# Optimization experiments

Measured on AMD Instinct MI355X. Metric: run time of the kernel, lower is better.

The kernel has to match this reference:

```python
import jax, jax.numpy as jnp
import numpy as np

B, CL, QL, D = 32, 1024, 512, 256


def setup_inputs() -> dict:
    key = jax.random.key(0)
    ks = jax.random.split(key, 8)
    c = jax.random.normal(ks[0], (B, CL, D), jnp.float32)
    q = jax.random.normal(ks[1], (B, QL, D), jnp.float32)
    scale = 1.0 / np.sqrt(D)
    w_c = jax.random.normal(ks[2], (D,), jnp.float32) * scale
    b_c = jax.random.normal(ks[3], (), jnp.float32) * 0.01
    w_q = jax.random.normal(ks[4], (D,), jnp.float32) * scale
    b_q = jax.random.normal(ks[5], (), jnp.float32) * 0.01
    w_cq = jax.random.normal(ks[6], (D,), jnp.float32) * scale
    b_cq = jax.random.normal(ks[7], (), jnp.float32) * 0.01
    return {"c": c, "q": q, "w_c": w_c, "b_c": b_c, "w_q": w_q, "b_q": b_q,
            "w_cq": w_cq, "b_cq": b_cq}


def reference(c, q, w_c, b_c, w_q, b_q, w_cq, b_cq):
    # s[b,i,j] = w_c.c_i + w_q.q_j + w_cq.(c_i*q_j) + biases
    sc = c @ w_c + b_c                                   # (B, CL)
    sq = q @ w_q + b_q                                   # (B, QL)
    # The original per-j loop att_weight_cq(c * q_j) is a batched bilinear form.
    cq = jnp.einsum('bid,bjd,d->bij', c, q, w_cq) + b_cq  # (B, CL, QL)
    s = sc[:, :, None] + sq[:, None, :] + cq              # (B, CL, QL)
    a = jax.nn.softmax(s, axis=2)
    c2q_att = jnp.einsum('bij,bjd->bid', a, q)            # (B, CL, D)
    bvec = jax.nn.softmax(jnp.max(s, axis=2), axis=1)     # (B, CL)
    q2c = jnp.einsum('bi,bid->bd', bvec, c)               # (B, D)
    q2c_att = jnp.broadcast_to(q2c[:, None, :], c.shape)  # (B, CL, D)
    x = jnp.concatenate([c, c2q_att, c * c2q_att, c * q2c_att], axis=-1)
    return x
```

## Files before the change

kernel.cpp:

```cpp
#include <hip/hip_runtime.h>

#define B_  32
#define CL_ 1024
#define QL_ 512
#define D_  256

typedef _Float16 f16;
typedef __attribute__((ext_vector_type(2))) _Float16 f16x2;
typedef __attribute__((ext_vector_type(4))) _Float16 f16x4;
typedef __attribute__((ext_vector_type(8))) _Float16 f16x8;
typedef __attribute__((ext_vector_type(4))) float    f32x4;

__global__ __launch_bounds__(256) void k0_prep(const float* __restrict__ q,
                                               const float* __restrict__ w_q,
                                               f16* __restrict__ q_h,
                                               f16* __restrict__ qT_h,
                                               float* __restrict__ sqv) {
  __shared__ f16 q_l[64][258];
  int b = blockIdx.y, j0 = blockIdx.x * 64, tid = threadIdx.x;
  int r = tid >> 2, seg = tid & 3;
  const float* qrow = q   + ((size_t)(b * QL_ + j0 + r)) * D_ + seg * 64;
  f16*        qhrow = q_h + ((size_t)(b * QL_ + j0 + r)) * D_ + seg * 64;
  float dot = 0.f;
  #pragma unroll
  for (int u = 0; u < 16; ++u) {
    f32x4 v  = *(const f32x4*)(qrow + 4 * u);
    f32x4 wv = *(const f32x4*)(w_q + seg * 64 + 4 * u);
    f16x4 h;
    h[0] = (f16)v[0]; h[1] = (f16)v[1]; h[2] = (f16)v[2]; h[3] = (f16)v[3];
    *(f16x4*)(&q_l[r][seg * 64 + 4 * u]) = h;
    *(f16x4*)(qhrow + 4 * u) = h;
    dot += v[0]*wv[0] + v[1]*wv[1] + v[2]*wv[2] + v[3]*wv[3];
  }
  dot += __shfl_xor(dot, 1, 64);
  dot += __shfl_xor(dot, 2, 64);
  if (seg == 0) sqv[b * QL_ + j0 + r] = dot;
  __syncthreads();
  f16* qTb = qT_h + (size_t)b * D_ * QL_ + j0;
  #pragma unroll
  for (int s = 0; s < 32; ++s) {
    int e = tid + 256 * s;
    int d = e >> 5, j2 = (e & 31) * 2;
    f16x2 p;
    p[0] = q_l[j2][d];
    p[1] = q_l[j2 + 1][d];
    *(f16x2*)(qTb + (size_t)d * QL_ + j2) = p;
  }
}

__global__ __launch_bounds__(512, 2) void k1_fused(
    const float* __restrict__ c, const f16* __restrict__ q_h,
    const f16* __restrict__ qT_h, const float* __restrict__ sqv,
    const float* __restrict__ w_c, const float* __restrict__ w_cq,
    float* __restrict__ out, float* __restrict__ mrow)
{
  __shared__ alignas(16) char smem[142848];
  f16 (*cw_t)[264]  = (f16 (*)[264])(smem);
  char* P_b         = smem;
  float (*o_l)[260] = (float (*)[260])(smem);
  float* sqv_l = (float*)(smem + 133120);
  float* wcq_l = (float*)(smem + 135168);
  float* wc_l  = (float*)(smem + 136192);
  float* scv_l = (float*)(smem + 137216);
  float (*red)[128] = (float (*)[128])(smem + 137728);
  float* mf = (float*)(smem + 141824);
  float* lf = (float*)(smem + 142336);

  const int tid = threadIdx.x;
  const int w = tid >> 6, l = tid & 63, g = l >> 4, l15 = l & 15;
  const int lin = blockIdx.x, xcd = lin & 7, slot = lin >> 3;
  const int b  = xcd * 4 + (slot >> 3);
  const int i0 = (slot & 7) * 128;

  if (tid < 256) { wcq_l[tid] = w_cq[tid]; wc_l[tid] = w_c[tid]; }
  sqv_l[tid] = sqv[b * QL_ + tid];
  __syncthreads();

  {
    int row = tid >> 2, seg = tid & 3;
    const float* crow = c + (size_t)(b * CL_ + i0 + row) * D_ + seg * 64;
    float dot = 0.f;
    #pragma unroll
    for (int u = 0; u < 16; ++u) {
      f32x4 v  = *(const f32x4*)(crow + 4 * u);
      f32x4 wv = *(const f32x4*)(wcq_l + seg * 64 + 4 * u);
      f32x4 w2 = *(const f32x4*)(wc_l  + seg * 64 + 4 * u);
      f16x4 h;
      h[0] = (f16)(v[0]*wv[0]); h[1] = (f16)(v[1]*wv[1]);
      h[2] = (f16)(v[2]*wv[2]); h[3] = (f16)(v[3]*wv[3]);
      *(f16x4*)(&cw_t[row][seg * 64 + 4 * u]) = h;
      dot += v[0]*w2[0] + v[1]*w2[1] + v[2]*w2[2] + v[3]*w2[3];
    }
    dot += __shfl_xor(dot, 1, 64); dot += __shfl_xor(dot, 2, 64);
    if (seg == 0) scv_l[row] = dot;
  }
  __syncthreads();

  f32x4 acc[8][4];
  #pragma unroll
  for (int fi = 0; fi < 8; ++fi)
    #pragma unroll
    for (int fj = 0; fj < 4; ++fj)
      acc[fi][fj] = (f32x4){0.f,0.f,0.f,0.f};

  const f16* qb = q_h + (size_t)b * QL_ * D_ + (size_t)(64 * w + l15) * D_ + 8 * g;
  #pragma unroll
  for (int dk = 0; dk < 8; ++dk) {
    f16x8 av[8];
    #pragma unroll
    for (int fi = 0; fi < 8; ++fi)
      av[fi] = *(const f16x8*)(&cw_t[16 * fi + l15][dk * 32 + 8 * g]);
    #pragma unroll
    for (int fj = 0; fj < 4; ++fj) {
      f16x8 bf = *(const f16x8*)(qb + (size_t)(16 * fj) * D_ + dk * 32);
      #pragma unroll
      for (int fi = 0; fi < 8; ++fi)
        acc[fi][fj] = __builtin_amdgcn_mfma_f32_16x16x32_f16(av[fi], bf, acc[fi][fj], 0, 0, 0);
    }
  }

  #pragma unroll
  for (int fi = 0; fi < 8; ++fi) {
    #pragma unroll
    for (int r = 0; r < 4; ++r) {
      float mx = -1e30f;
      #pragma unroll
      for (int fj = 0; fj < 4; ++fj) {
        float v = acc[fi][fj][r] + sqv_l[64 * w + 16 * fj + l15];
        acc[fi][fj][r] = v;
        mx = fmaxf(mx, v);
      }
      mx = fmaxf(mx, __shfl_xor(mx, 1, 64));
      mx = fmaxf(mx, __shfl_xor(mx, 2, 64));
      mx = fmaxf(mx, __shfl_xor(mx, 4, 64));
      mx = fmaxf(mx, __shfl_xor(mx, 8, 64));
      if (l15 == 0) red[w][16 * fi + 4 * g + r] = mx;
    }
  }
  __syncthreads();
  if (tid < 128) {
    float m = red[0][tid];
    #pragma unroll
    for (int w2 = 1; w2 < 8; ++w2) m = fmaxf(m, red[w2][tid]);
    mf[tid] = m;
    mrow[b * CL_ + i0 + tid] = m + scv_l[tid];
  }
  __syncthreads();
  #pragma unroll
  for (int fi = 0; fi < 8; ++fi) {
    #pragma unroll
    for (int r = 0; r < 4; ++r) {
      float mv = mf[16 * fi + 4 * g + r];
      float s = 0.f;
      #pragma unroll
      for (int fj = 0; fj < 4; ++fj) {
        float p = __expf(acc[fi][fj][r] - mv);
        acc[fi][fj][r] = p;
        s += p;
      }
      s += __shfl_xor(s, 1, 64); s += __shfl_xor(s, 2, 64);
      s += __shfl_xor(s, 4, 64); s += __shfl_xor(s, 8, 64);
      if (l15 == 0) red[w][16 * fi + 4 * g + r] = s;
    }
  }
  __syncthreads();
  if (tid < 128) {
    float s = 0.f;
    #pragma unroll
    for (int w2 = 0; w2 < 8; ++w2) s += red[w2][tid];
    lf[tid] = 1.0f / s;
  }
  __syncthreads();

  #pragma unroll
  for (int fi = 0; fi < 8; ++fi) {
    #pragma unroll
    for (int r = 0; r < 4; ++r) {
      int row = 16 * fi + 4 * g + r;
      float inv = lf[row];
      int rb = (row << 10) ^ ((row & 7) << 4);
      #pragma unroll
      for (int fj = 0; fj < 4; ++fj) {
        int byte = (rb ^ ((128 * w + 32 * fj + 2 * l15) & 0x70))
                 | ((128 * w + 32 * fj + 2 * l15) & ~0x70);
        *(f16*)(P_b + (((row << 10) + 128 * w + 32 * fj + 2 * l15) ^ ((row & 7) << 4)))
            = (f16)(acc[fi][fj][r] * inv);
        (void)byte;
      }
    }
  }
  __syncthreads();

  f32x4 o[8][2];
  #pragma unroll
  for (int fi = 0; fi < 8; ++fi) { o[fi][0] = (f32x4){0.f,0.f,0.f,0.f}; o[fi][1] = o[fi][0]; }
  const f16* qTb = qT_h + (size_t)b * D_ * QL_ + (size_t)(32 * w + l15) * QL_ + 8 * g;
  #pragma unroll
  for (int jt = 0; jt < 16; ++jt) {
    f16x8 qf0 = *(const f16x8*)(qTb + jt * 32);
    f16x8 qf1 = *(const f16x8*)(qTb + 16 * QL_ + jt * 32);
    #pragma unroll
    for (int fi = 0; fi < 8; ++fi) {
      int row = 16 * fi + l15;
      f16x8 pa = *(const f16x8*)(P_b + (((row << 10) + 64 * jt + 16 * g) ^ ((row & 7) << 4)));
      o[fi][0] = __builtin_amdgcn_mfma_f32_16x16x32_f16(pa, qf0, o[fi][0], 0, 0, 0);
      o[fi][1] = __builtin_amdgcn_mfma_f32_16x16x32_f16(pa, qf1, o[fi][1], 0, 0, 0);
    }
  }
  __syncthreads();

  #pragma unroll
  for (int fi = 0; fi < 8; ++fi)
    #pragma unroll
    for (int fd = 0; fd < 2; ++fd)
      #pragma unroll
      for (int r = 0; r < 4; ++r)
        o_l[16 * fi + 4 * g + r][32 * w + 16 * fd + l15] = o[fi][fd][r];
  __syncthreads();

  #pragma unroll
  for (int s = 0; s < 16; ++s) {
    int idx = tid + 512 * s;
    int row = idx >> 6, c4 = (idx & 63) * 4;
    size_t rowoff = (size_t)(b * CL_ + i0 + row);
    f32x4 c2q = *(const f32x4*)(&o_l[row][c4]);
    f32x4 cv  = *(const f32x4*)(c + rowoff * D_ + c4);
    f32x4 prod;
    prod[0] = cv[0]*c2q[0]; prod[1] = cv[1]*c2q[1];
    prod[2] = cv[2]*c2q[2]; prod[3] = cv[3]*c2q[3];
    float* ob = out + rowoff * (4 * D_) + c4;
    *(f32x4*)(ob)          = cv;
    *(f32x4*)(ob + D_)     = c2q;
    *(f32x4*)(ob + 2 * D_) = prod;
  }
}

__global__ __launch_bounds__(256) void k2a_bvec(const float* __restrict__ mrow,
                                                float* __restrict__ bvec) {
  __shared__ float red[256];
  int b = blockIdx.x, tid = threadIdx.x;
  f32x4 v = *(const f32x4*)(mrow + b * CL_ + tid * 4);
  float mx = fmaxf(fmaxf(v[0], v[1]), fmaxf(v[2], v[3]));
  red[tid] = mx;
  __syncthreads();
  for (int s = 128; s > 0; s >>= 1) {
    if (tid < s) red[tid] = fmaxf(red[tid], red[tid + s]);
    __syncthreads();
  }
  float gmx = red[0];
  __syncthreads();
  f32x4 e;
  e[0] = __expf(v[0] - gmx); e[1] = __expf(v[1] - gmx);
  e[2] = __expf(v[2] - gmx); e[3] = __expf(v[3] - gmx);
  red[tid] = e[0] + e[1] + e[2] + e[3];
  __syncthreads();
  for (int s = 128; s > 0; s >>= 1) {
    if (tid < s) red[tid] += red[tid + s];
    __syncthreads();
  }
  float inv = 1.0f / red[0];
  e[0] *= inv; e[1] *= inv; e[2] *= inv; e[3] *= inv;
  *(f32x4*)(bvec + b * CL_ + tid * 4) = e;
}

__global__ __launch_bounds__(256) void k2b_part(const float* __restrict__ c,
                                                const float* __restrict__ bvec,
                                                float* __restrict__ part) {
  __shared__ f32x4 pl[4][64];
  int ch = blockIdx.x, b = blockIdx.y, tid = threadIdx.x;
  int ro = tid >> 6, dl = tid & 63;
  const float* cb = c + ((size_t)b * CL_ + ch * 128) * D_;
  const float* bv = bvec + b * CL_ + ch * 128;
  f32x4 acc = (f32x4){0.f, 0.f, 0.f, 0.f};
  for (int i = ro; i < 128; i += 4) {
    float wgt = bv[i];
    f32x4 v = *(const f32x4*)(cb + (size_t)i * D_ + dl * 4);
    acc[0] += wgt * v[0]; acc[1] += wgt * v[1];
    acc[2] += wgt * v[2]; acc[3] += wgt * v[3];
  }
  pl[ro][dl] = acc;
  __syncthreads();
  if (tid < 64) {
    f32x4 s = (pl[0][tid] + pl[1][tid]) + (pl[2][tid] + pl[3][tid]);
    *(f32x4*)(part + ((size_t)(b * 8 + ch)) * D_ + tid * 4) = s;
  }
}

__global__ __launch_bounds__(256) void k2c_red(const float* __restrict__ part,
                                               float* __restrict__ q2c) {
  int b = blockIdx.x, d = threadIdx.x;
  float s = 0.f;
  #pragma unroll
  for (int ch = 0; ch < 8; ++ch) s += part[((size_t)(b * 8 + ch)) * D_ + d];
  q2c[b * D_ + d] = s;
}

__global__ __launch_bounds__(256) void k3_tail(const float* __restrict__ c,
                                               const float* __restrict__ q2c,
                                               float* __restrict__ out) {
  size_t idx = (size_t)blockIdx.x * 256 + threadIdx.x;
  int b   = (int)(idx >> 16);
  int rem = (int)(idx & 65535);
  int i = rem >> 6, d4 = (rem & 63) * 4;
  f32x4 cv = *(const f32x4*)(c + (size_t)(b * CL_ + i) * D_ + d4);
  f32x4 gv = *(const f32x4*)(q2c + b * D_ + d4);
  f32x4 r;
  r[0] = cv[0]*gv[0]; r[1] = cv[1]*gv[1]; r[2] = cv[2]*gv[2]; r[3] = cv[3]*gv[3];
  *(f32x4*)(out + (size_t)(b * CL_ + i) * (4 * D_) + 3 * D_ + d4) = r;
}

extern "C" void kernel_launch(void* const* d_in, const int* in_sizes, int n_in,
                              void* d_out, int out_size, void* d_ws, size_t ws_size,
                              hipStream_t stream) {
  const float* c    = (const float*)d_in[0];
  const float* q    = (const float*)d_in[1];
  const float* w_c  = (const float*)d_in[2];
  const float* w_q  = (const float*)d_in[4];
  const float* w_cq = (const float*)d_in[6];
  float* out = (float*)d_out;
  char* ws = (char*)d_ws;
  f16*   q_h  = (f16*)ws;
  f16*   qT_h = (f16*)(ws + 8388608);
  float* sqv  = (float*)(ws + 16777216);
  float* mrow = (float*)(ws + 16842752);
  float* bvec = (float*)(ws + 16973824);
  float* part = (float*)(ws + 17104896);
  float* q2c  = (float*)(ws + 17367040);

  hipLaunchKernelGGL(k0_prep,  dim3(8, 32),  dim3(256), 0, stream,
                     q, w_q, q_h, qT_h, sqv);
  hipLaunchKernelGGL(k1_fused, dim3(256),    dim3(512), 0, stream,
                     c, q_h, qT_h, sqv, w_c, w_cq, out, mrow);
  hipLaunchKernelGGL(k2a_bvec, dim3(32),     dim3(256), 0, stream, mrow, bvec);
  hipLaunchKernelGGL(k2b_part, dim3(8, 32),  dim3(256), 0, stream, c, bvec, part);
  hipLaunchKernelGGL(k2c_red,  dim3(32),     dim3(256), 0, stream, part, q2c);
  hipLaunchKernelGGL(k3_tail,  dim3(8192),   dim3(256), 0, stream, c, q2c, out);
}
```

Baseline: 99.55 us.

## Stage q chunks through swizzled LDS for the score GEMM

The first GEMM used to read q fragments straight from global memory, each wave pulling its own 64-column slice. It now loads q in four 128-row chunks cooperatively into a swizzled LDS buffer and has all waves read B fragments from LDS. The column assignment is reorganised to match (jc chunks, 16 columns per wave per chunk), and the P write indexing is updated. The aim is coalesced global loads and shorter global-load latency in the MFMA loop. In exchange it adds two barriers per chunk, re-reads the A operand from LDS for every chunk, and does not overlap loads with compute.

```diff
diff --git a/kernel.cpp b/kernel.cpp
--- a/kernel.cpp
+++ b/kernel.cpp
@@ -56,6 +56,7 @@
 {
   __shared__ alignas(16) char smem[142848];
   f16 (*cw_t)[264]  = (f16 (*)[264])(smem);
+  char* qA          = smem + 67584;
   char* P_b         = smem;
   float (*o_l)[260] = (float (*)[260])(smem);
   float* sqv_l = (float*)(smem + 133120);
@@ -94,29 +95,37 @@
     dot += __shfl_xor(dot, 1, 64); dot += __shfl_xor(dot, 2, 64);
     if (seg == 0) scv_l[row] = dot;
   }
-  __syncthreads();
-
-  f32x4 acc[8][4];
-  #pragma unroll
-  for (int fi = 0; fi < 8; ++fi)
-    #pragma unroll
-    for (int fj = 0; fj < 4; ++fj)
-      acc[fi][fj] = (f32x4){0.f,0.f,0.f,0.f};
-
-  const f16* qb = q_h + (size_t)b * QL_ * D_ + (size_t)(64 * w + l15) * D_ + 8 * g;
-  #pragma unroll
-  for (int dk = 0; dk < 8; ++dk) {
-    f16x8 av[8];
+
+  f32x4 acc[4][8];
+  #pragma unroll
+  for (int jc = 0; jc < 4; ++jc)
     #pragma unroll
     for (int fi = 0; fi < 8; ++fi)
-      av[fi] = *(const f16x8*)(&cw_t[16 * fi + l15][dk * 32 + 8 * g]);
-    #pragma unroll
-    for (int fj = 0; fj < 4; ++fj) {
-      f16x8 bf = *(const f16x8*)(qb + (size_t)(16 * fj) * D_ + dk * 32);
-      #pragma unroll
-      for (int fi = 0; fi < 8; ++fi)
-        acc[fi][fj] = __builtin_amdgcn_mfma_f32_16x16x32_f16(av[fi], bf, acc[fi][fj], 0, 0, 0);
-    }
+      acc[jc][fi] = (f32x4){0.f,0.f,0.f,0.f};
+
+  const char* qhbC = (const char*)(q_h + (size_t)b * QL_ * D_);
+  const int jrow = 16 * w + l15, jsw = jrow & 7;
+  #pragma unroll
+  for (int jc = 0; jc < 4; ++jc) {
+    const char* src = qhbC + (size_t)jc * 65536;
+    #pragma unroll
+    for (int s = 0; s < 8; ++s) {
+      int idx = s * 512 + tid;
+      int row = idx >> 5, sl = idx & 31;
+      f32x4 v = *(const f32x4*)(src + (size_t)idx * 16);
+      *(f32x4*)(qA + row * 512 + ((sl ^ (row & 7)) << 4)) = v;
+    }
+    __syncthreads();
+    #pragma unroll
+    for (int dk = 0; dk < 8; ++dk) {
+      f16x8 bf = *(const f16x8*)(qA + jrow * 512 + (((dk * 4 + g) ^ jsw) << 4));
+      #pragma unroll
+      for (int fi = 0; fi < 8; ++fi) {
+        f16x8 av = *(const f16x8*)(&cw_t[16 * fi + l15][dk * 32 + 8 * g]);
+        acc[jc][fi] = __builtin_amdgcn_mfma_f32_16x16x32_f16(av, bf, acc[jc][fi], 0, 0, 0);
+      }
+    }
+    __syncthreads();
   }
 
   #pragma unroll
@@ -125,9 +134,9 @@
     for (int r = 0; r < 4; ++r) {
       float mx = -1e30f;
       #pragma unroll
-      for (int fj = 0; fj < 4; ++fj) {
-        float v = acc[fi][fj][r] + sqv_l[64 * w + 16 * fj + l15];
-        acc[fi][fj][r] = v;
+      for (int jc = 0; jc < 4; ++jc) {
+        float v = acc[jc][fi][r] + sqv_l[jc * 128 + 16 * w + l15];
+        acc[jc][fi][r] = v;
         mx = fmaxf(mx, v);
       }
       mx = fmaxf(mx, __shfl_xor(mx, 1, 64));
@@ -153,9 +162,9 @@
       float mv = mf[16 * fi + 4 * g + r];
       float s = 0.f;
       #pragma unroll
-      for (int fj = 0; fj < 4; ++fj) {
-        float p = __expf(acc[fi][fj][r] - mv);
-        acc[fi][fj][r] = p;
+      for (int jc = 0; jc < 4; ++jc) {
+        float p = __expf(acc[jc][fi][r] - mv);
+        acc[jc][fi][r] = p;
         s += p;
       }
       s += __shfl_xor(s, 1, 64); s += __shfl_xor(s, 2, 64);
@@ -178,14 +187,10 @@
     for (int r = 0; r < 4; ++r) {
       int row = 16 * fi + 4 * g + r;
       float inv = lf[row];
-      int rb = (row << 10) ^ ((row & 7) << 4);
-      #pragma unroll
-      for (int fj = 0; fj < 4; ++fj) {
-        int byte = (rb ^ ((128 * w + 32 * fj + 2 * l15) & 0x70))
-                 | ((128 * w + 32 * fj + 2 * l15) & ~0x70);
-        *(f16*)(P_b + (((row << 10) + 128 * w + 32 * fj + 2 * l15) ^ ((row & 7) << 4)))
-            = (f16)(acc[fi][fj][r] * inv);
-        (void)byte;
+      #pragma unroll
+      for (int jc = 0; jc < 4; ++jc) {
+        *(f16*)(P_b + (((row << 10) + jc * 256 + 32 * w + 2 * l15) ^ ((row & 7) << 4)))
+            = (f16)(acc[jc][fi][r] * inv);
       }
     }
   }
```

Result: slower. 104.2 us (+4.7%).
